# Performance work log

Measured on AMD Instinct MI355X. Metric: run time of the kernel, lower is better.

## Reference

```python
import jax, jax.numpy as jnp
import numpy as np


def _conv1x1(x, w, b):
    # x: [B,C,H,W], w: [O,C], b: [O]  (1x1 conv == per-pixel matmul)
    return jnp.einsum('bchw,oc->bohw', x, w) + b[None, :, None, None]


def setup_inputs() -> dict:
    key = jax.random.key(0)
    ks = jax.random.split(key, 9)
    B, C, H, W = 4, 64, 64, 64
    Ch = C // 2
    s_in = 1.0 / np.sqrt(C)
    s_h = 1.0 / np.sqrt(Ch)
    return {
        'x': jax.random.normal(ks[0], (B, C, H, W), dtype=jnp.float32),
        'w1': jax.random.normal(ks[1], (Ch, C), dtype=jnp.float32) * s_in,
        'b1': jax.random.normal(ks[2], (Ch,), dtype=jnp.float32) * s_in,
        'w2': jax.random.normal(ks[3], (Ch, C), dtype=jnp.float32) * s_in,
        'b2': jax.random.normal(ks[4], (Ch,), dtype=jnp.float32) * s_in,
        'w3': jax.random.normal(ks[5], (Ch, C), dtype=jnp.float32) * s_in,
        'b3': jax.random.normal(ks[6], (Ch,), dtype=jnp.float32) * s_in,
        'w4': jax.random.normal(ks[7], (C, Ch), dtype=jnp.float32) * s_h,
        'b4': jax.random.normal(ks[8], (C,), dtype=jnp.float32) * s_h,
    }


def reference(x, w1, b1, w2, b2, w3, b3, w4, b4):
    B, C, H, W = x.shape
    N = H * W
    # NOTE: original torch code does .view (raw reshape) with NO permute,
    # so channel/spatial axes get mixed exactly as in the source.
    x1 = _conv1x1(x, w1, b1).reshape(B, N, -1)   # [B, N, C/2] (raw reshape)
    x2 = _conv1x1(x, w2, b2).reshape(B, -1, N)   # [B, C/2, N]
    attn = jnp.matmul(x1, x2)                    # [B, N, N]
    # F.softmax with no dim on a 3D tensor -> legacy implicit dim = 0 (batch)
    attn = jax.nn.softmax(attn, axis=0)
    y = _conv1x1(x, w3, b3).reshape(B, N, -1)    # [B, N, C/2]
    y = jnp.matmul(attn, y)                      # [B, N, C/2]
    y = y.reshape(B, -1, H, W)                   # [B, C/2, H, W]
    return _conv1x1(y, w4, b4)                   # [B, C, H, W]
```

## Files before the change

### kernel.cpp

```cpp
#include <hip/hip_runtime.h>


typedef _Float16 half8 __attribute__((ext_vector_type(8)));
typedef _Float16 half4 __attribute__((ext_vector_type(4)));
typedef float f32x4 __attribute__((ext_vector_type(4)));

#define N_PIX 4096
#define NB    4
#define JS    32
#define LOG2E 1.44269504088896f

__global__ __launch_bounds__(256) void convs_kernel(
    const float* __restrict__ x,
    const float* __restrict__ w1, const float* __restrict__ b1,
    const float* __restrict__ w2, const float* __restrict__ b2,
    const float* __restrict__ w3, const float* __restrict__ b3,
    _Float16* __restrict__ X1h, _Float16* __restrict__ X2f, _Float16* __restrict__ Y3f)
{
    const int t = blockIdx.y;
    const float* __restrict__ w  = (t == 0) ? w1 : ((t == 1) ? w2 : w3);
    const float* __restrict__ bb = (t == 0) ? b1 : ((t == 1) ? b2 : b3);

    __shared__ float sw[8][64];
    __shared__ float sbias[8];
    __shared__ _Float16 sbuf[2048];

    const int tid   = threadIdx.x;
    const int b     = blockIdx.x >> 6;
    const int chunk = (blockIdx.x >> 2) & 15;
    const int og    = blockIdx.x & 3;
    const int o0    = og * 8;
    const int hw    = chunk * 256 + tid;

    for (int e = tid; e < 8 * 64; e += 256)
        sw[e >> 6][e & 63] = w[(o0 + (e >> 6)) * 64 + (e & 63)];
    if (tid < 8) sbias[tid] = bb[o0 + tid];
    __syncthreads();

    float xi[64];
    const float* xb = x + b * 64 * N_PIX + hw;
    #pragma unroll
    for (int c = 0; c < 64; c++) xi[c] = xb[c * N_PIX];

    float acc[8];
    #pragma unroll
    for (int oo = 0; oo < 8; oo++) {
        float a0 = sbias[oo], a1 = 0.f, a2 = 0.f, a3 = 0.f;
        #pragma unroll
        for (int c = 0; c < 64; c += 4) {
            a0 += xi[c + 0] * sw[oo][c + 0];
            a1 += xi[c + 1] * sw[oo][c + 1];
            a2 += xi[c + 2] * sw[oo][c + 2];
            a3 += xi[c + 3] * sw[oo][c + 3];
        }
        acc[oo] = (a0 + a1) + (a2 + a3);
    }

    if (t == 0) {
        #pragma unroll
        for (int oo = 0; oo < 8; oo++)
            X1h[b * 131072 + (o0 + oo) * N_PIX + hw] = (_Float16)(acc[oo] * LOG2E);
    } else if (t == 1) {
        #pragma unroll
        for (int oo = 0; oo < 8; oo++)
            sbuf[tid * 8 + oo] = (_Float16)acc[oo];
        __syncthreads();
        const int m    = tid & 15;
        const int jh   = (tid >> 4) & 1;
        const int jt_l = (tid >> 5) & 7;
        const int jl   = jt_l * 32 + ((m >> 2) * 8) + (m & 3) + jh * 4;
        half8 v = *(half8*)&sbuf[jl * 8];
        *(half8*)&X2f[(((b * 128 + chunk * 8 + jt_l) * 2 + jh) * 64 + og * 16 + m) * 8] = v;
    } else {
        const int c  = tid & 31;
        const int jl = tid >> 5;
        #pragma unroll
        for (int oo = 0; oo < 8; oo++)
            sbuf[(oo * 32 + c) * 8 + jl] = (_Float16)acc[oo];
        __syncthreads();
        const int m  = tid & 15;
        const int ch = (tid >> 4) & 1;
        const int oo = (tid >> 5) & 7;
        half8 v = *(half8*)&sbuf[(oo * 32 + ch * 16 + m) * 8];
        const int jt = (o0 + oo) * 4 + (chunk >> 2);
        *(half8*)&Y3f[(((b * 128 + jt) * 2 + ch) * 64 + (chunk & 3) * 16 + m) * 8] = v;
    }
}

__global__ __launch_bounds__(256) void attn_kernel(
    const _Float16* __restrict__ X1h, const _Float16* __restrict__ X2f,
    const _Float16* __restrict__ Y3f, _Float16* __restrict__ OPh)
{
    __shared__ _Float16 sRedH[4 * 64 * 36];

    const int tid  = threadIdx.x;
    const int wv   = tid >> 6;
    const int lane = tid & 63;
    const int m    = lane & 15;
    const int q    = lane >> 4;
    const int i0   = blockIdx.x * 16;
    const int js   = blockIdx.y;
    const int jg   = js * 4 + wv;

    half8 bx1[NB];
    #pragma unroll
    for (int b = 0; b < NB; b++)
        bx1[b] = *(const half8*)&X1h[b * 131072 + (i0 + m) * 32 + q * 8];

    half8 ax2[NB][2], ay3[NB][2];
    #pragma unroll
    for (int b = 0; b < NB; b++) {
        #pragma unroll
        for (int jh = 0; jh < 2; jh++)
            ax2[b][jh] = *(const half8*)&X2f[(((b * 128 + jg) * 2 + jh) * 64 + lane) * 8];
        #pragma unroll
        for (int ch = 0; ch < 2; ch++)
            ay3[b][ch] = *(const half8*)&Y3f[(((b * 128 + jg) * 2 + ch) * 64 + lane) * 8];
    }

    f32x4 sT[NB][2];
    #pragma unroll
    for (int b = 0; b < NB; b++)
        #pragma unroll
        for (int jh = 0; jh < 2; jh++)
            sT[b][jh] = __builtin_amdgcn_mfma_f32_16x16x32_f16(
                ax2[b][jh], bx1[b], (f32x4){0.f, 0.f, 0.f, 0.f}, 0, 0, 0);

    half8 pf[NB];
    #pragma unroll
    for (int jh = 0; jh < 2; jh++)
        #pragma unroll
        for (int r = 0; r < 4; r++) {
            float e0 = exp2f(sT[0][jh][r]);
            float e1 = exp2f(sT[1][jh][r]);
            float e2 = exp2f(sT[2][jh][r]);
            float e3 = exp2f(sT[3][jh][r]);
            float rs = __builtin_amdgcn_rcpf(e0 + e1 + e2 + e3);
            pf[0][jh * 4 + r] = (_Float16)(e0 * rs);
            pf[1][jh * 4 + r] = (_Float16)(e1 * rs);
            pf[2][jh * 4 + r] = (_Float16)(e2 * rs);
            pf[3][jh * 4 + r] = (_Float16)(e3 * rs);
        }

    f32x4 oaccT[NB][2];
    #pragma unroll
    for (int b = 0; b < NB; b++)
        #pragma unroll
        for (int ch = 0; ch < 2; ch++)
            oaccT[b][ch] = __builtin_amdgcn_mfma_f32_16x16x32_f16(
                ay3[b][ch], pf[b], (f32x4){0.f, 0.f, 0.f, 0.f}, 0, 0, 0);

    #pragma unroll
    for (int b = 0; b < NB; b++)
        #pragma unroll
        for (int ch = 0; ch < 2; ch++) {
            half4 h;
            #pragma unroll
            for (int r = 0; r < 4; r++) h[r] = (_Float16)oaccT[b][ch][r];
            *(half4*)&sRedH[(wv * 64 + lane) * 36 + b * 8 + ch * 4] = h;
        }
    __syncthreads();

    const int bb = tid >> 6;
    const int lp = tid & 63;
    const int mm = lp & 15;
    const int qq = lp >> 4;
    #pragma unroll
    for (int ch = 0; ch < 2; ch++) {
        half4 h0 = *(half4*)&sRedH[(0 * 64 + lp) * 36 + bb * 8 + ch * 4];
        half4 h1 = *(half4*)&sRedH[(1 * 64 + lp) * 36 + bb * 8 + ch * 4];
        half4 h2 = *(half4*)&sRedH[(2 * 64 + lp) * 36 + bb * 8 + ch * 4];
        half4 h3 = *(half4*)&sRedH[(3 * 64 + lp) * 36 + bb * 8 + ch * 4];
        half4 v;
        #pragma unroll
        for (int r = 0; r < 4; r++)
            v[r] = (_Float16)(((float)h0[r] + (float)h1[r]) + ((float)h2[r] + (float)h3[r]));
        *(half4*)&OPh[js * 524288 + (bb * 4096 + i0 + mm) * 32 + ch * 16 + qq * 4] = v;
    }
}

__global__ __launch_bounds__(256) void reduce_out_kernel(
    const _Float16* __restrict__ OPh, const float* __restrict__ w4,
    const float* __restrict__ b4, float* __restrict__ out)
{
    __shared__ float sY[32 * 72];
    __shared__ float sw[64 * 32];
    __shared__ float sbias[64];

    const int tid = threadIdx.x;
    for (int e = tid; e < 64 * 32; e += 256) sw[e] = w4[e];
    if (tid < 64) sbias[tid] = b4[tid];

    const int b   = blockIdx.x >> 6;
    const int hw0 = (blockIdx.x & 63) * 64;

    const int ch    = tid >> 3;
    const int piece = tid & 7;
    {
        float acc[8] = {};
        const _Float16* base = OPh + b * 131072 + ch * 4096 + hw0 + piece * 8;
        #pragma unroll
        for (int p = 0; p < JS; p++) {
            half8 v = *(const half8*)&base[p * 524288];
            #pragma unroll
            for (int e = 0; e < 8; e++) acc[e] += (float)v[e];
        }
        *(f32x4*)&sY[ch * 72 + piece * 8]     = (f32x4){acc[0], acc[1], acc[2], acc[3]};
        *(f32x4*)&sY[ch * 72 + piece * 8 + 4] = (f32x4){acc[4], acc[5], acc[6], acc[7]};
    }
    __syncthreads();

    const int hw_l = tid & 63;
    const int og   = tid >> 6;

    float y2[32];
    #pragma unroll
    for (int c = 0; c < 32; c++) y2[c] = sY[c * 72 + hw_l];

    float* obp = out + b * 64 * N_PIX + hw0 + hw_l;
    #pragma unroll
    for (int oo = 0; oo < 16; oo++) {
        const int o = og * 16 + oo;
        float a0 = sbias[o], a1 = 0.f, a2 = 0.f, a3 = 0.f;
        #pragma unroll
        for (int c = 0; c < 32; c += 4) {
            a0 += y2[c + 0] * sw[o * 32 + c + 0];
            a1 += y2[c + 1] * sw[o * 32 + c + 1];
            a2 += y2[c + 2] * sw[o * 32 + c + 2];
            a3 += y2[c + 3] * sw[o * 32 + c + 3];
        }
        obp[o * N_PIX] = (a0 + a1) + (a2 + a3);
    }
}

extern "C" void kernel_launch(void* const* d_in, const int* in_sizes, int n_in,
                              void* d_out, int out_size, void* d_ws, size_t ws_size,
                              hipStream_t stream) {
    const float* x  = (const float*)d_in[0];
    const float* w1 = (const float*)d_in[1];
    const float* b1 = (const float*)d_in[2];
    const float* w2 = (const float*)d_in[3];
    const float* b2 = (const float*)d_in[4];
    const float* w3 = (const float*)d_in[5];
    const float* b3 = (const float*)d_in[6];
    const float* w4 = (const float*)d_in[7];
    const float* b4 = (const float*)d_in[8];

    char* wsb = (char*)d_ws;
    _Float16* X1h = (_Float16*)(wsb);
    _Float16* X2f = (_Float16*)(wsb + (1 << 20));
    _Float16* Y3f = (_Float16*)(wsb + (2 << 20));
    _Float16* OPh = (_Float16*)(wsb + (3 << 20));
    float*    out = (float*)d_out;

    dim3 g1(256, 3);
    convs_kernel<<<g1, 256, 0, stream>>>(x, w1, b1, w2, b2, w3, b3, X1h, X2f, Y3f);
    dim3 g2(256, JS);
    attn_kernel<<<g2, 256, 0, stream>>>(X1h, X2f, Y3f, OPh);
    reduce_out_kernel<<<256, 256, 0, stream>>>(OPh, w4, b4, out);
}
```

Before: 130.0 us.

## Loop attention blocks over eight i-tiles to reuse X2/Y3 register fragments

Each attention block now handles 8 consecutive 16-row i-tiles in a loop instead of one, so the per-wave X2 and Y3 fragments loaded from global memory are reused across iterations. The grid shrinks from 256 to 32 blocks in x. The next tile's X1 fragment is prefetched while the current one computes, and the shared reduction buffer is double-buffered so a single barrier per iteration is enough. The cost is fewer blocks (1024 total) and less parallelism to hide latency, plus extra LDS and registers.

```diff
diff --git a/kernel.cpp b/kernel.cpp
--- a/kernel.cpp
+++ b/kernel.cpp
@@ -8,6 +8,7 @@
 #define N_PIX 4096
 #define NB    4
 #define JS    32
+#define IT    8
 #define LOG2E 1.44269504088896f
 
 __global__ __launch_bounds__(256) void convs_kernel(
@@ -91,22 +92,17 @@
     const _Float16* __restrict__ X1h, const _Float16* __restrict__ X2f,
     const _Float16* __restrict__ Y3f, _Float16* __restrict__ OPh)
 {
-    __shared__ _Float16 sRedH[4 * 64 * 36];
+    __shared__ _Float16 sRedH[2][4 * 64 * 36];
 
     const int tid  = threadIdx.x;
     const int wv   = tid >> 6;
     const int lane = tid & 63;
     const int m    = lane & 15;
     const int q    = lane >> 4;
-    const int i0   = blockIdx.x * 16;
+    const int ig   = blockIdx.x;
     const int js   = blockIdx.y;
     const int jg   = js * 4 + wv;
 
-    half8 bx1[NB];
-    #pragma unroll
-    for (int b = 0; b < NB; b++)
-        bx1[b] = *(const half8*)&X1h[b * 131072 + (i0 + m) * 32 + q * 8];
-
     half8 ax2[NB][2], ay3[NB][2];
     #pragma unroll
     for (int b = 0; b < NB; b++) {
@@ -118,64 +114,79 @@
             ay3[b][ch] = *(const half8*)&Y3f[(((b * 128 + jg) * 2 + ch) * 64 + lane) * 8];
     }
 
-    f32x4 sT[NB][2];
+    half8 nbx1[NB];
     #pragma unroll
     for (int b = 0; b < NB; b++)
+        nbx1[b] = *(const half8*)&X1h[b * 131072 + (ig * 128 + m) * 32 + q * 8];
+
+    #pragma unroll 2
+    for (int it = 0; it < IT; it++) {
+        half8 bx1[NB];
+        #pragma unroll
+        for (int b = 0; b < NB; b++) bx1[b] = nbx1[b];
+        if (it + 1 < IT) {
+            #pragma unroll
+            for (int b = 0; b < NB; b++)
+                nbx1[b] = *(const half8*)&X1h[b * 131072 + (ig * 128 + (it + 1) * 16 + m) * 32 + q * 8];
+        }
+
+        f32x4 sT[NB][2];
+        #pragma unroll
+        for (int b = 0; b < NB; b++)
+            #pragma unroll
+            for (int jh = 0; jh < 2; jh++)
+                sT[b][jh] = __builtin_amdgcn_mfma_f32_16x16x32_f16(
+                    ax2[b][jh], bx1[b], (f32x4){0.f, 0.f, 0.f, 0.f}, 0, 0, 0);
+
+        half8 pf[NB];
         #pragma unroll
         for (int jh = 0; jh < 2; jh++)
-            sT[b][jh] = __builtin_amdgcn_mfma_f32_16x16x32_f16(
-                ax2[b][jh], bx1[b], (f32x4){0.f, 0.f, 0.f, 0.f}, 0, 0, 0);
-
-    half8 pf[NB];
-    #pragma unroll
-    for (int jh = 0; jh < 2; jh++)
-        #pragma unroll
-        for (int r = 0; r < 4; r++) {
-            float e0 = exp2f(sT[0][jh][r]);
-            float e1 = exp2f(sT[1][jh][r]);
-            float e2 = exp2f(sT[2][jh][r]);
-            float e3 = exp2f(sT[3][jh][r]);
-            float rs = __builtin_amdgcn_rcpf(e0 + e1 + e2 + e3);
-            pf[0][jh * 4 + r] = (_Float16)(e0 * rs);
-            pf[1][jh * 4 + r] = (_Float16)(e1 * rs);
-            pf[2][jh * 4 + r] = (_Float16)(e2 * rs);
-            pf[3][jh * 4 + r] = (_Float16)(e3 * rs);
-        }
-
-    f32x4 oaccT[NB][2];
-    #pragma unroll
-    for (int b = 0; b < NB; b++)
-        #pragma unroll
-        for (int ch = 0; ch < 2; ch++)
-            oaccT[b][ch] = __builtin_amdgcn_mfma_f32_16x16x32_f16(
-                ay3[b][ch], pf[b], (f32x4){0.f, 0.f, 0.f, 0.f}, 0, 0, 0);
-
-    #pragma unroll
-    for (int b = 0; b < NB; b++)
+            #pragma unroll
+            for (int r = 0; r < 4; r++) {
+                float e0 = exp2f(sT[0][jh][r]);
+                float e1 = exp2f(sT[1][jh][r]);
+                float e2 = exp2f(sT[2][jh][r]);
+                float e3 = exp2f(sT[3][jh][r]);
+                float rs = __builtin_amdgcn_rcpf(e0 + e1 + e2 + e3);
+                pf[0][jh * 4 + r] = (_Float16)(e0 * rs);
+                pf[1][jh * 4 + r] = (_Float16)(e1 * rs);
+                pf[2][jh * 4 + r] = (_Float16)(e2 * rs);
+                pf[3][jh * 4 + r] = (_Float16)(e3 * rs);
+            }
+
+        f32x4 oaccT[NB][2];
+        #pragma unroll
+        for (int b = 0; b < NB; b++)
+            #pragma unroll
+            for (int ch = 0; ch < 2; ch++)
+                oaccT[b][ch] = __builtin_amdgcn_mfma_f32_16x16x32_f16(
+                    ay3[b][ch], pf[b], (f32x4){0.f, 0.f, 0.f, 0.f}, 0, 0, 0);
+
+        const int p = it & 1;
+        #pragma unroll
+        for (int b = 0; b < NB; b++)
+            #pragma unroll
+            for (int ch = 0; ch < 2; ch++) {
+                half4 h;
+                #pragma unroll
+                for (int r = 0; r < 4; r++) h[r] = (_Float16)oaccT[b][ch][r];
+                *(half4*)&sRedH[p][(wv * 64 + lane) * 36 + b * 8 + ch * 4] = h;
+            }
+        __syncthreads();
+
+        const int i0 = ig * 128 + it * 16;
         #pragma unroll
         for (int ch = 0; ch < 2; ch++) {
-            half4 h;
-            #pragma unroll
-            for (int r = 0; r < 4; r++) h[r] = (_Float16)oaccT[b][ch][r];
-            *(half4*)&sRedH[(wv * 64 + lane) * 36 + b * 8 + ch * 4] = h;
-        }
-    __syncthreads();
-
-    const int bb = tid >> 6;
-    const int lp = tid & 63;
-    const int mm = lp & 15;
-    const int qq = lp >> 4;
-    #pragma unroll
-    for (int ch = 0; ch < 2; ch++) {
-        half4 h0 = *(half4*)&sRedH[(0 * 64 + lp) * 36 + bb * 8 + ch * 4];
-        half4 h1 = *(half4*)&sRedH[(1 * 64 + lp) * 36 + bb * 8 + ch * 4];
-        half4 h2 = *(half4*)&sRedH[(2 * 64 + lp) * 36 + bb * 8 + ch * 4];
-        half4 h3 = *(half4*)&sRedH[(3 * 64 + lp) * 36 + bb * 8 + ch * 4];
-        half4 v;
-        #pragma unroll
-        for (int r = 0; r < 4; r++)
-            v[r] = (_Float16)(((float)h0[r] + (float)h1[r]) + ((float)h2[r] + (float)h3[r]));
-        *(half4*)&OPh[js * 524288 + (bb * 4096 + i0 + mm) * 32 + ch * 16 + qq * 4] = v;
+            half4 h0 = *(half4*)&sRedH[p][(0 * 64 + lane) * 36 + wv * 8 + ch * 4];
+            half4 h1 = *(half4*)&sRedH[p][(1 * 64 + lane) * 36 + wv * 8 + ch * 4];
+            half4 h2 = *(half4*)&sRedH[p][(2 * 64 + lane) * 36 + wv * 8 + ch * 4];
+            half4 h3 = *(half4*)&sRedH[p][(3 * 64 + lane) * 36 + wv * 8 + ch * 4];
+            half4 v;
+            #pragma unroll
+            for (int r = 0; r < 4; r++)
+                v[r] = (_Float16)(((float)h0[r] + (float)h1[r]) + ((float)h2[r] + (float)h3[r]));
+            *(half4*)&OPh[js * 524288 + (wv * 4096 + i0 + m) * 32 + ch * 16 + q * 4] = v;
+        }
     }
 }
 
@@ -255,7 +266,7 @@
 
     dim3 g1(256, 3);
     convs_kernel<<<g1, 256, 0, stream>>>(x, w1, b1, w2, b2, w3, b3, X1h, X2f, Y3f);
-    dim3 g2(256, JS);
+    dim3 g2(32, JS);
     attn_kernel<<<g2, 256, 0, stream>>>(X1h, X2f, Y3f, OPh);
     reduce_out_kernel<<<256, 256, 0, stream>>>(OPh, w4, b4, out);
 }
```

Result: no change. 131.2 us (+0.9%).
